# Kernel tuning notes

Hardware: AMD Instinct MI355X
Metric: run time of the kernel (lower is better)

Reference implementation:

```python
import jax, jax.numpy as jnp
import numpy as np

B, S, D, U = 32, 4096, 512, 128

def setup_inputs() -> dict:
    key = jax.random.key(0)
    k1, k2, k3, k4, k5 = jax.random.split(key, 5)
    query = jax.random.normal(k1, (B, D), dtype=jnp.float32)
    values = jax.random.normal(k2, (B, S, D), dtype=jnp.float32)
    s = 1.0 / np.sqrt(D)
    W1 = jax.random.normal(k3, (D, U), dtype=jnp.float32) * s
    W2 = jax.random.normal(k4, (D, U), dtype=jnp.float32) * s
    V = jax.random.normal(k5, (U, 1), dtype=jnp.float32) * (1.0 / np.sqrt(U))
    b1 = jnp.zeros((U,), dtype=jnp.float32)
    b2 = jnp.zeros((U,), dtype=jnp.float32)
    bv = jnp.zeros((1,), dtype=jnp.float32)
    return {"query": query, "values": values, "W1": W1, "b1": b1,
            "W2": W2, "b2": b2, "V": V, "bv": bv}

def reference(query, values, W1, b1, W2, b2, V, bv):
    # query: [B, D] -> [B, 1, U]; values: [B, S, D] -> [B, S, U]
    q_proj = (query @ W1 + b1)[:, None, :]                  # [B, 1, U]
    v_proj = jnp.einsum('bsd,du->bsu', values, W2) + b2      # [B, S, U]
    score = jnp.tanh(q_proj + v_proj) @ V + bv               # [B, S, 1]
    attention_weights = jax.nn.softmax(score, axis=1)        # [B, S, 1]
    context_vector = jnp.sum(attention_weights * values, axis=1)  # [B, D]
    return context_vector, attention_weights
```

## Files before the change

kernel.cpp:

```cpp
#include <hip/hip_runtime.h>
#include <math.h>

#define NB 32
#define NS 4096
#define ND 512
#define NU 128
#define RR 32
#define ASTR 520

typedef __bf16 bf16x8 __attribute__((ext_vector_type(8)));
typedef unsigned short u16x8 __attribute__((ext_vector_type(8)));
typedef float f32x4 __attribute__((ext_vector_type(4)));

union FragCvt { u16x8 u; bf16x8 b; };

__device__ inline unsigned short f2bf(float x) {
  union { float f; unsigned u; } v; v.f = x;
  return (unsigned short)((v.u + 0x7FFFu + ((v.u >> 16) & 1u)) >> 16);
}
__device__ inline float bf2f(unsigned int bits16) {
  union { unsigned u; float f; } v; v.u = bits16 << 16;
  return v.f;
}
__device__ inline float fast_tanh(float x) {
  x = fminf(9.f, fmaxf(-9.f, x));
  float e2 = __expf(2.f * x);
  return (e2 - 1.f) * __builtin_amdgcn_rcpf(e2 + 1.f);
}

__global__ void prep_qb(const float* __restrict__ q, const float* __restrict__ W1,
                        const float* __restrict__ b1, const float* __restrict__ b2,
                        float* __restrict__ qb) {
  const int bb = blockIdx.x >> 4;
  const int kc = blockIdx.x & 15;
  const int u  = threadIdx.x & 127;
  const int dh = threadIdx.x >> 7;
  const int d0 = kc * 32 + dh * 16;
  const float* qr = q + bb * ND + d0;
  const float* w  = W1 + (size_t)d0 * NU + u;
  float s = (kc == 0 && dh == 0) ? (b1[u] + b2[u]) : 0.f;
  #pragma unroll
  for (int j = 0; j < 16; ++j) s += qr[j] * w[j * NU];
  atomicAdd(qb + bb * NU + u, s);
}

__global__ void prep_w2f(const float* __restrict__ W2, uint4* __restrict__ w2f) {
  const int idx = blockIdx.x * 256 + threadIdx.x;
  const int lane = idx & 63;
  const int ut   = (idx >> 6) & 7;
  const int kt   = idx >> 9;
  const int lidx = lane & 15;
  const int quad = lane >> 4;
  const int u  = ut * 16 + lidx;
  const int d0 = kt * 32 + quad * 8;
  unsigned short o[8];
  #pragma unroll
  for (int j = 0; j < 8; ++j) o[j] = f2bf(W2[(size_t)(d0 + j) * NU + u]);
  w2f[idx] = *(const uint4*)o;
}

__global__ __launch_bounds__(256, 4) void fused_attn(
    const float* __restrict__ values,
    const float* __restrict__ qb,
    const uint4* __restrict__ w2f,
    const float* __restrict__ V,
    const float* __restrict__ bvp,
    float* __restrict__ wout,
    float* __restrict__ Cacc,
    float* __restrict__ Lacc)
{
  __shared__ unsigned short Alds[RR * ASTR];
  __shared__ float sbuf[4][16];
  __shared__ float wlds[RR];

  const int tid = threadIdx.x;
  const int b = blockIdx.x >> 7;
  const int chunk = blockIdx.x & 127;
  const int s0 = chunk * RR;

  const float* vbase = values + ((size_t)b * NS + s0) * ND;
  #pragma unroll
  for (int ii = 0; ii < 16; ii += 8) {
    float4 v[8];
    #pragma unroll
    for (int j = 0; j < 8; ++j) {
      const int f = tid + 256 * (ii + j);
      v[j] = *(const float4*)(vbase + (f >> 7) * ND + (f & 127) * 4);
    }
    #pragma unroll
    for (int j = 0; j < 8; ++j) {
      const int f = tid + 256 * (ii + j);
      ushort4 pk;
      pk.x = f2bf(v[j].x); pk.y = f2bf(v[j].y); pk.z = f2bf(v[j].z); pk.w = f2bf(v[j].w);
      *(ushort4*)(&Alds[(f >> 7) * ASTR + (f & 127) * 4]) = pk;
    }
  }
  __syncthreads();

  const int wave = tid >> 6, lane = tid & 63;
  const int quad = lane >> 4, lidx = lane & 15;
  const int mtile = wave & 1;
  const int nbase = (wave >> 1) * 64;
  const int utb = (wave >> 1) * 4;

  f32x4 acc[4] = {{0.f,0.f,0.f,0.f},{0.f,0.f,0.f,0.f},{0.f,0.f,0.f,0.f},{0.f,0.f,0.f,0.f}};
  const unsigned short* arow = &Alds[(mtile * 16 + lidx) * ASTR];
  const uint4* wfl = w2f + lane;

  #pragma unroll 4
  for (int kt = 0; kt < 16; ++kt) {
    FragCvt af; af.u = *(const u16x8*)(arow + kt * 32 + quad * 8);
    #pragma unroll
    for (int nt = 0; nt < 4; ++nt) {
      FragCvt bf; bf.u = *(const u16x8*)(wfl + (kt * 8 + utb + nt) * 64);
      acc[nt] = __builtin_amdgcn_mfma_f32_16x16x32_bf16(af.b, bf.b, acc[nt], 0, 0, 0);
    }
  }

  float part[4] = {0.f, 0.f, 0.f, 0.f};
  #pragma unroll
  for (int nt = 0; nt < 4; ++nt) {
    const int col = nbase + nt * 16 + lidx;
    const float qv = qb[b * NU + col];
    const float vv = V[col];
    #pragma unroll
    for (int r = 0; r < 4; ++r)
      part[r] += fast_tanh(acc[nt][r] + qv) * vv;
  }
  #pragma unroll
  for (int m = 1; m <= 8; m <<= 1) {
    #pragma unroll
    for (int r = 0; r < 4; ++r) part[r] += __shfl_xor(part[r], m, 64);
  }
  if (lidx == 0) {
    #pragma unroll
    for (int r = 0; r < 4; ++r) sbuf[wave][quad * 4 + r] = part[r];
  }
  __syncthreads();

  if (tid < 32) {
    const int mt = tid >> 4, rr = tid & 15;
    float s = sbuf[mt][rr] + sbuf[mt + 2][rr];
    float e = __expf(s + *bvp);
    wout[(size_t)b * NS + s0 + tid] = e;
    wlds[tid] = e;
    float es = e;
    #pragma unroll
    for (int m = 1; m <= 16; m <<= 1) es += __shfl_xor(es, m, 64);
    if (tid == 0) atomicAdd(Lacc + b, es);
  }
  __syncthreads();

  const int d0 = tid * 2;
  float c0 = 0.f, c1 = 0.f;
  #pragma unroll 8
  for (int r = 0; r < RR; ++r) {
    const float w = wlds[r];
    const unsigned int pk = *(const unsigned int*)(&Alds[r * ASTR + d0]);
    c0 += w * bf2f(pk & 0xFFFFu);
    c1 += w * bf2f(pk >> 16);
  }
  atomicAdd(Cacc + b * ND + d0, c0);
  atomicAdd(Cacc + b * ND + d0 + 1, c1);
}

__global__ void finalize(const float* __restrict__ Cacc, const float* __restrict__ Lacc,
                         float* __restrict__ out) {
  int idx = blockIdx.x * 256 + threadIdx.x;
  if (idx < NB * ND) {
    int b = idx >> 9;
    out[idx] = Cacc[idx] / Lacc[b];
  } else {
    int j = idx - NB * ND;
    int b = j >> 12;
    out[idx] = out[idx] / Lacc[b];
  }
}

extern "C" void kernel_launch(void* const* d_in, const int* in_sizes, int n_in,
                              void* d_out, int out_size, void* d_ws, size_t ws_size,
                              hipStream_t stream) {
  const float* query  = (const float*)d_in[0];
  const float* values = (const float*)d_in[1];
  const float* W1     = (const float*)d_in[2];
  const float* b1     = (const float*)d_in[3];
  const float* W2     = (const float*)d_in[4];
  const float* b2     = (const float*)d_in[5];
  const float* V      = (const float*)d_in[6];
  const float* bv     = (const float*)d_in[7];
  float* out = (float*)d_out;

  char* ws = (char*)d_ws;
  float* Cacc = (float*)ws;
  float* Lacc = (float*)(ws + 65536);
  float* qb   = (float*)(ws + 66048);
  uint4* w2f  = (uint4*)(ws + 66048 + 16384);

  hipMemsetAsync(ws, 0, 66048 + 16384, stream);

  prep_qb <<<NB * 16, 256, 0, stream>>>(query, W1, b1, b2, qb);
  prep_w2f<<<32, 256, 0, stream>>>(W2, w2f);
  fused_attn<<<NB * (NS / RR), 256, 0, stream>>>(values, qb, w2f, V, bv,
                                                 out + NB * ND, Cacc, Lacc);
  finalize<<<(NB * ND + NB * NS) / 256, 256, 0, stream>>>(Cacc, Lacc, out);
}
```

Before: 426.4 us.

## Load MFMA A-fragments directly from global memory instead of staging values in LDS

Removes the shared-memory staging of the 32x512 values tile. Each wave now loads its A fragments straight from global memory and converts them to bf16 in registers. The context accumulation re-reads the fp32 values from global memory, relying on cache reuse. This frees about 33KB of LDS per block and removes a barrier, aiming for higher occupancy. The cost is less coalesced fragment loads and a second global read of the tile.

```diff
diff --git a/kernel.cpp b/kernel.cpp
--- a/kernel.cpp
+++ b/kernel.cpp
@@ -6,7 +6,6 @@
 #define ND 512
 #define NU 128
 #define RR 32
-#define ASTR 520
 
 typedef __bf16 bf16x8 __attribute__((ext_vector_type(8)));
 typedef unsigned short u16x8 __attribute__((ext_vector_type(8)));
@@ -17,10 +16,6 @@
 __device__ inline unsigned short f2bf(float x) {
   union { float f; unsigned u; } v; v.f = x;
   return (unsigned short)((v.u + 0x7FFFu + ((v.u >> 16) & 1u)) >> 16);
-}
-__device__ inline float bf2f(unsigned int bits16) {
-  union { unsigned u; float f; } v; v.u = bits16 << 16;
-  return v.f;
 }
 __device__ inline float fast_tanh(float x) {
   x = fminf(9.f, fmaxf(-9.f, x));
@@ -69,7 +64,6 @@
     float* __restrict__ Cacc,
     float* __restrict__ Lacc)
 {
-  __shared__ unsigned short Alds[RR * ASTR];
   __shared__ float sbuf[4][16];
   __shared__ float wlds[RR];
 
@@ -78,38 +72,26 @@
   const int chunk = blockIdx.x & 127;
   const int s0 = chunk * RR;
 
-  const float* vbase = values + ((size_t)b * NS + s0) * ND;
-  #pragma unroll
-  for (int ii = 0; ii < 16; ii += 8) {
-    float4 v[8];
-    #pragma unroll
-    for (int j = 0; j < 8; ++j) {
-      const int f = tid + 256 * (ii + j);
-      v[j] = *(const float4*)(vbase + (f >> 7) * ND + (f & 127) * 4);
-    }
-    #pragma unroll
-    for (int j = 0; j < 8; ++j) {
-      const int f = tid + 256 * (ii + j);
-      ushort4 pk;
-      pk.x = f2bf(v[j].x); pk.y = f2bf(v[j].y); pk.z = f2bf(v[j].z); pk.w = f2bf(v[j].w);
-      *(ushort4*)(&Alds[(f >> 7) * ASTR + (f & 127) * 4]) = pk;
-    }
-  }
-  __syncthreads();
-
   const int wave = tid >> 6, lane = tid & 63;
   const int quad = lane >> 4, lidx = lane & 15;
   const int mtile = wave & 1;
   const int nbase = (wave >> 1) * 64;
   const int utb = (wave >> 1) * 4;
 
-  f32x4 acc[4] = {{0.f,0.f,0.f,0.f},{0.f,0.f,0.f,0.f},{0.f,0.f,0.f,0.f},{0.f,0.f,0.f,0.f}};
-  const unsigned short* arow = &Alds[(mtile * 16 + lidx) * ASTR];
+  const float4* arow4 = (const float4*)(values + ((size_t)b * NS + s0 + mtile * 16 + lidx) * ND);
   const uint4* wfl = w2f + lane;
 
-  #pragma unroll 4
+  f32x4 acc[4] = {{0.f,0.f,0.f,0.f},{0.f,0.f,0.f,0.f},{0.f,0.f,0.f,0.f},{0.f,0.f,0.f,0.f}};
+
+  #pragma unroll 2
   for (int kt = 0; kt < 16; ++kt) {
-    FragCvt af; af.u = *(const u16x8*)(arow + kt * 32 + quad * 8);
+    float4 a0 = arow4[kt * 8 + quad * 2];
+    float4 a1 = arow4[kt * 8 + quad * 2 + 1];
+    FragCvt af;
+    af.b[0] = (__bf16)a0.x; af.b[1] = (__bf16)a0.y;
+    af.b[2] = (__bf16)a0.z; af.b[3] = (__bf16)a0.w;
+    af.b[4] = (__bf16)a1.x; af.b[5] = (__bf16)a1.y;
+    af.b[6] = (__bf16)a1.z; af.b[7] = (__bf16)a1.w;
     #pragma unroll
     for (int nt = 0; nt < 4; ++nt) {
       FragCvt bf; bf.u = *(const u16x8*)(wfl + (kt * 8 + utb + nt) * 64);
@@ -151,15 +133,16 @@
   }
   __syncthreads();
 
-  const int d0 = tid * 2;
+  const float* vb2 = values + ((size_t)b * NS + s0) * ND + tid * 2;
   float c0 = 0.f, c1 = 0.f;
   #pragma unroll 8
   for (int r = 0; r < RR; ++r) {
     const float w = wlds[r];
-    const unsigned int pk = *(const unsigned int*)(&Alds[r * ASTR + d0]);
-    c0 += w * bf2f(pk & 0xFFFFu);
-    c1 += w * bf2f(pk >> 16);
+    const float2 v = *(const float2*)(vb2 + r * ND);
+    c0 += w * v.x;
+    c1 += w * v.y;
   }
+  const int d0 = tid * 2;
   atomicAdd(Cacc + b * ND + d0, c0);
   atomicAdd(Cacc + b * ND + d0 + 1, c1);
 }
```

New measurement: 443.0 us. 3.9% more time.

## Stage W2 fragments through swizzled double-buffered LDS instead of direct global loads

Applied to the files above, without the earlier changes.

W2 is now stored as plain bf16 tiles ([kt][u][k]). Each k-tile is loaded cooperatively into registers, written into a double-buffered, XOR-swizzled LDS region, and prefetched one tile ahead. MFMA B fragments are then read from LDS. Before, each wave pulled fragment-ordered data directly from global/L2. The goal is to cut redundant per-wave global traffic for W2. In exchange, each block now pays 16 __syncthreads and extra LDS usage, and launch bounds drop to 3 blocks per CU.

```diff
diff --git a/kernel.cpp b/kernel.cpp
--- a/kernel.cpp
+++ b/kernel.cpp
@@ -27,6 +27,7 @@
   float e2 = __expf(2.f * x);
   return (e2 - 1.f) * __builtin_amdgcn_rcpf(e2 + 1.f);
 }
+__device__ inline int bswz(int byte) { return byte ^ (((byte >> 7) & 7) << 4); }
 
 __global__ void prep_qb(const float* __restrict__ q, const float* __restrict__ W1,
                         const float* __restrict__ b1, const float* __restrict__ b2,
@@ -44,25 +45,18 @@
   atomicAdd(qb + bb * NU + u, s);
 }
 
-__global__ void prep_w2f(const float* __restrict__ W2, uint4* __restrict__ w2f) {
+__global__ void prep_w2s(const float* __restrict__ W2, unsigned short* __restrict__ w2s) {
   const int idx = blockIdx.x * 256 + threadIdx.x;
-  const int lane = idx & 63;
-  const int ut   = (idx >> 6) & 7;
-  const int kt   = idx >> 9;
-  const int lidx = lane & 15;
-  const int quad = lane >> 4;
-  const int u  = ut * 16 + lidx;
-  const int d0 = kt * 32 + quad * 8;
-  unsigned short o[8];
-  #pragma unroll
-  for (int j = 0; j < 8; ++j) o[j] = f2bf(W2[(size_t)(d0 + j) * NU + u]);
-  w2f[idx] = *(const uint4*)o;
-}
-
-__global__ __launch_bounds__(256, 4) void fused_attn(
+  const int u = idx & 127;
+  const int r = idx >> 7;
+  const int k = r & 31, kt = r >> 5;
+  w2s[kt * 4096 + u * 32 + k] = f2bf(W2[(size_t)(kt * 32 + k) * NU + u]);
+}
+
+__global__ __launch_bounds__(256, 3) void fused_attn(
     const float* __restrict__ values,
     const float* __restrict__ qb,
-    const uint4* __restrict__ w2f,
+    const unsigned short* __restrict__ w2s,
     const float* __restrict__ V,
     const float* __restrict__ bvp,
     float* __restrict__ wout,
@@ -70,6 +64,7 @@
     float* __restrict__ Lacc)
 {
   __shared__ unsigned short Alds[RR * ASTR];
+  __shared__ unsigned short Blds[2][128 * 32];
   __shared__ float sbuf[4][16];
   __shared__ float wlds[RR];
 
@@ -77,6 +72,10 @@
   const int b = blockIdx.x >> 7;
   const int chunk = blockIdx.x & 127;
   const int s0 = chunk * RR;
+
+  const uint4* w2s4 = (const uint4*)w2s;
+  uint4 breg0 = w2s4[tid * 2];
+  uint4 breg1 = w2s4[tid * 2 + 1];
 
   const float* vbase = values + ((size_t)b * NS + s0) * ND;
   #pragma unroll
@@ -95,24 +94,31 @@
       *(ushort4*)(&Alds[(f >> 7) * ASTR + (f & 127) * 4]) = pk;
     }
   }
-  __syncthreads();
 
   const int wave = tid >> 6, lane = tid & 63;
   const int quad = lane >> 4, lidx = lane & 15;
   const int mtile = wave & 1;
   const int nbase = (wave >> 1) * 64;
-  const int utb = (wave >> 1) * 4;
 
   f32x4 acc[4] = {{0.f,0.f,0.f,0.f},{0.f,0.f,0.f,0.f},{0.f,0.f,0.f,0.f},{0.f,0.f,0.f,0.f}};
   const unsigned short* arow = &Alds[(mtile * 16 + lidx) * ASTR];
-  const uint4* wfl = w2f + lane;
-
-  #pragma unroll 4
+
   for (int kt = 0; kt < 16; ++kt) {
+    char* bdst = (char*)Blds[kt & 1];
+    const int by0 = tid * 32;
+    *(uint4*)(bdst + bswz(by0))      = breg0;
+    *(uint4*)(bdst + bswz(by0 + 16)) = breg1;
+    __syncthreads();
+    if (kt < 15) {
+      breg0 = w2s4[(kt + 1) * 512 + tid * 2];
+      breg1 = w2s4[(kt + 1) * 512 + tid * 2 + 1];
+    }
     FragCvt af; af.u = *(const u16x8*)(arow + kt * 32 + quad * 8);
+    const char* bsrc = (const char*)Blds[kt & 1];
     #pragma unroll
     for (int nt = 0; nt < 4; ++nt) {
-      FragCvt bf; bf.u = *(const u16x8*)(wfl + (kt * 8 + utb + nt) * 64);
+      const int bb2 = (nbase + nt * 16 + lidx) * 64 + quad * 16;
+      FragCvt bf; bf.u = *(const u16x8*)(bsrc + bswz(bb2));
       acc[nt] = __builtin_amdgcn_mfma_f32_16x16x32_bf16(af.b, bf.b, acc[nt], 0, 0, 0);
     }
   }
@@ -194,13 +200,13 @@
   float* Cacc = (float*)ws;
   float* Lacc = (float*)(ws + 65536);
   float* qb   = (float*)(ws + 66048);
-  uint4* w2f  = (uint4*)(ws + 66048 + 16384);
+  unsigned short* w2s = (unsigned short*)(ws + 66048 + 16384);
 
   hipMemsetAsync(ws, 0, 66048 + 16384, stream);
 
   prep_qb <<<NB * 16, 256, 0, stream>>>(query, W1, b1, b2, qb);
-  prep_w2f<<<32, 256, 0, stream>>>(W2, w2f);
-  fused_attn<<<NB * (NS / RR), 256, 0, stream>>>(values, qb, w2f, V, bv,
+  prep_w2s<<<256, 256, 0, stream>>>(W2, w2s);
+  fused_attn<<<NB * (NS / RR), 256, 0, stream>>>(values, qb, w2s, V, bv,
                                                  out + NB * ND, Cacc, Lacc);
   finalize<<<(NB * ND + NB * NS) / 256, 256, 0, stream>>>(Cacc, Lacc, out);
 }
```

Measured after the change: 412.7 us. 3.2% less time.
